# Kernel optimization log

Hardware: AMD Instinct MI355X
Metric: run time of the kernel (lower is better)

The kernel has to match this reference:

```python
import jax, jax.numpy as jnp
import numpy as np
import math

P_PARTICLES = 50
N_ITERS = 30
ROT_RANGE = math.radians(45.0)
TR_RANGE = 1.0
F_DE = 0.8
CR_DE = 0.9
SUB = 128


def axis_angle_to_rotation_matrix(v):
    # v: [..., 3] axis-angle -> [..., 3, 3] via Rodrigues formula
    theta = jnp.linalg.norm(v, axis=-1, keepdims=True)            # [..., 1]
    k = v / jnp.maximum(theta, 1e-8)
    kx, ky, kz = k[..., 0], k[..., 1], k[..., 2]
    zero = jnp.zeros_like(kx)
    K = jnp.stack([zero, -kz, ky,
                   kz, zero, -kx,
                   -ky, kx, zero], axis=-1).reshape(v.shape[:-1] + (3, 3))
    I = jnp.eye(3, dtype=v.dtype)
    s = jnp.sin(theta)[..., None]
    c = jnp.cos(theta)[..., None]
    R = I + s * K + (1.0 - c) * (K @ K)
    return jnp.where(theta[..., None] < 1e-8, I, R)


def _evaluate(src, tgt, pop):
    # src: [B,S,3] subsampled source, tgt: [B,S,3], pop: [B,P,6]
    R = axis_angle_to_rotation_matrix(pop[..., :3])               # [B,P,3,3]
    t = pop[..., 3:]                                              # [B,P,3]
    # transformed[b,p,n,k] = sum_j src[b,n,j] * R[b,p,k,j] + t[b,p,k]
    x = jnp.einsum('bnj,bpkj->bpnk', src, R) + t[:, :, None, :]   # [B,P,S,3]
    # squared-distance chamfer (symmetric, mean of nearest-neighbor dists)
    xn = jnp.sum(x * x, axis=-1)                                  # [B,P,S]
    yn = jnp.sum(tgt * tgt, axis=-1)                              # [B,S]
    cross = jnp.einsum('bpnd,bmd->bpnm', x, tgt)                  # [B,P,S,S]
    d2 = jnp.maximum(xn[..., None] + yn[:, None, None, :] - 2.0 * cross, 0.0)
    return d2.min(axis=-1).mean(axis=-1) + d2.min(axis=-2).mean(axis=-1)  # [B,P]


def setup_inputs() -> dict:
    key = jax.random.key(0)
    k1, k2 = jax.random.split(key)
    source = jax.random.normal(k1, (32, 16384, 3), dtype=jnp.float32)
    target = jax.random.normal(k2, (32, 16384, 3), dtype=jnp.float32)
    return {"source": source, "target": target}


def reference(source, target):
    B, N, _ = source.shape
    M = target.shape[1]
    P = P_PARTICLES
    key = jax.random.key(42)
    k0, k1, k2, k3, kloop = jax.random.split(key, 5)

    # subsample points for fitness evaluation (shared indices across batch)
    idx_s = jax.random.permutation(k0, N)[:SUB]
    idx_t = jax.random.permutation(k1, M)[:SUB]
    src = source[:, idx_s, :]                                     # [B,S,3]
    tgt = target[:, idx_t, :]                                     # [B,S,3]

    # init population: uniform axis-angle + translation; particle 0 = identity
    rot = jax.random.uniform(k2, (B, P, 3), minval=-ROT_RANGE, maxval=ROT_RANGE)
    tr = jax.random.uniform(k3, (B, P, 3), minval=-TR_RANGE, maxval=TR_RANGE)
    pop = jnp.concatenate([rot, tr], axis=-1).at[:, 0, :].set(0.0)
    fit = _evaluate(src, tgt, pop)                                # [B,P]

    dim_ids = jnp.arange(6)

    def step(carry, k):
        pop, fit = carry
        ka, kb, kc = jax.random.split(k, 3)
        # per-batch random permutations of particle indices (r1, r2, r3)
        perm_keys = jax.random.split(ka, 3 * B)
        perms = jax.vmap(lambda kk: jax.random.permutation(kk, P))(perm_keys)
        perms = perms.reshape(3, B, P)

        def gather(r):
            return jnp.take_along_axis(pop, r[..., None], axis=1)  # [B,P,6]

        x1, x2, x3 = gather(perms[0]), gather(perms[1]), gather(perms[2])
        mutant = x1 + F_DE * (x2 - x3)
        mutant = jnp.concatenate([
            jnp.clip(mutant[..., :3], -ROT_RANGE, ROT_RANGE),
            jnp.clip(mutant[..., 3:], -TR_RANGE, TR_RANGE),
        ], axis=-1)

        rmask = jax.random.uniform(kb, (B, P, 6)) < CR_DE
        j_rand = jax.random.randint(kc, (B, P), 0, 6)
        cross_mask = rmask | (dim_ids == j_rand[..., None])
        trial = jnp.where(cross_mask, mutant, pop)

        tfit = _evaluate(src, tgt, trial)
        improved = tfit < fit
        pop = jnp.where(improved[..., None], trial, pop)
        fit = jnp.where(improved, tfit, fit)
        return (pop, fit), None

    (pop, fit), _ = jax.lax.scan(step, (pop, fit), jax.random.split(kloop, N_ITERS))

    best_idx = jnp.argmin(fit, axis=1)                            # [B]
    best_pos = pop[jnp.arange(B), best_idx]                       # [B,6]
    R_best = axis_angle_to_rotation_matrix(best_pos[:, :3])       # [B,3,3]
    t_best = best_pos[:, 3:]                                      # [B,3]
    aligned = jnp.einsum('bnj,bkj->bnk', source, R_best) + t_best[:, None, :]
    return (R_best, t_best, aligned)
```

## Files before the change

kernel.cpp:

```cpp
#include <hip/hip_runtime.h>
#include <stdint.h>

struct U2 { unsigned a, b; };

__device__ __forceinline__ unsigned rotl32(unsigned v, int r) {
  return (v << r) | (v >> (32 - r));
}

__device__ __forceinline__ U2 tf(U2 k, unsigned x0, unsigned x1) {
  unsigned ks0 = k.a, ks1 = k.b, ks2 = k.a ^ k.b ^ 0x1BD11BDAu;
  x0 += ks0; x1 += ks1;
#define TFG(RA, RB, RC, RD, KA, KB, INC)                  \
  x0 += x1; x1 = rotl32(x1, RA); x1 ^= x0;                \
  x0 += x1; x1 = rotl32(x1, RB); x1 ^= x0;                \
  x0 += x1; x1 = rotl32(x1, RC); x1 ^= x0;                \
  x0 += x1; x1 = rotl32(x1, RD); x1 ^= x0;                \
  x0 += KA; x1 += KB + INC;
  TFG(13, 15, 26, 6, ks1, ks2, 1u)
  TFG(17, 29, 16, 24, ks2, ks0, 2u)
  TFG(13, 15, 26, 6, ks0, ks1, 3u)
  TFG(17, 29, 16, 24, ks1, ks2, 4u)
  TFG(13, 15, 26, 6, ks2, ks0, 5u)
#undef TFG
  U2 r; r.a = x0; r.b = x1; return r;
}

__device__ __forceinline__ U2 split_key(U2 key, int num, int j) {
  (void)num;
  return tf(key, 0u, (unsigned)j);
}
__device__ __forceinline__ unsigned random_bits(U2 key, int n, unsigned e) {
  (void)n;
  U2 r = tf(key, 0u, e);
  return r.a ^ r.b;
}

__device__ __forceinline__ U2 root_key() { U2 k; k.a = 0u; k.b = 42u; return k; }

__device__ __forceinline__ float jax_uniform(U2 key, int n, unsigned e,
                                             float minv, float maxv) {
  unsigned b = random_bits(key, n, e);
  float u = __uint_as_float((b >> 9) | 0x3f800000u) - 1.0f;
  float r = u * (maxv - minv) + minv;
  return fmaxf(minv, r);
}

#define ROTR 0.7853981633974483f
#define SENTINEL 0xFFFFFFFFu

__device__ __forceinline__ void compute_R(float vx, float vy, float vz,
                                          float R[3][3]) {
  float nsq = vx * vx + vy * vy + vz * vz;
  float theta = sqrtf(nsq);
  if (theta < 1e-8f) {
    R[0][0] = 1.f; R[0][1] = 0.f; R[0][2] = 0.f;
    R[1][0] = 0.f; R[1][1] = 1.f; R[1][2] = 0.f;
    R[2][0] = 0.f; R[2][1] = 0.f; R[2][2] = 1.f;
    return;
  }
  float m = fmaxf(theta, 1e-8f);
  float kx = vx / m, ky = vy / m, kz = vz / m;
  float s = sinf(theta), c = cosf(theta);
  float K[3][3] = {{0.f, -kz, ky}, {kz, 0.f, -kx}, {-ky, kx, 0.f}};
  float K2[3][3];
#pragma unroll
  for (int i = 0; i < 3; i++)
#pragma unroll
    for (int j = 0; j < 3; j++)
      K2[i][j] = fmaf(K[i][2], K[2][j], fmaf(K[i][1], K[1][j], K[i][0] * K[0][j]));
  float omc = 1.0f - c;
#pragma unroll
  for (int i = 0; i < 3; i++)
#pragma unroll
    for (int j = 0; j < 3; j++)
      R[i][j] = ((i == j) ? 1.0f : 0.0f) + s * K[i][j] + omc * K2[i][j];
}

__device__ __forceinline__ unsigned long long make_composite(int s, int i) {
  U2 root = root_key();
  U2 kp = split_key(root, 5, s >> 1);
  U2 key;
  if ((s & 1) == 0) {
    key = split_key(kp, 2, 1);
  } else {
    U2 kA = split_key(kp, 2, 0);
    key = split_key(kA, 2, 1);
  }
  unsigned rb = random_bits(key, 16384, (unsigned)i);
  return ((unsigned long long)rb << 32) | (unsigned)i;
}

__device__ __forceinline__ float gload(const float* p) {
  return __hip_atomic_load(const_cast<float*>(p), __ATOMIC_RELAXED,
                           __HIP_MEMORY_SCOPE_AGENT);
}
__device__ __forceinline__ void gstore(float* p, float v) {
  __hip_atomic_store(p, v, __ATOMIC_RELAXED, __HIP_MEMORY_SCOPE_AGENT);
}
__device__ __forceinline__ unsigned uload(const unsigned* p) {
  return __hip_atomic_load(const_cast<unsigned*>(p), __ATOMIC_RELAXED,
                           __HIP_MEMORY_SCOPE_AGENT);
}

__device__ __forceinline__ float poll_word(const float* p) {
  const unsigned* up = (const unsigned*)p;
  unsigned v = uload(up);
  while (v == SENTINEL) v = uload(up);
  return __uint_as_float(v);
}

__global__ __launch_bounds__(256) void hist_kernel(unsigned* __restrict__ hist) {
  int gid = blockIdx.x * 256 + threadIdx.x;
  int s = gid >> 14, i = gid & 16383;
  unsigned long long c = make_composite(s, i);
  unsigned bucket = (unsigned)(c >> 56);
  atomicAdd(&hist[s * 256 + bucket], 1u);
}

__global__ __launch_bounds__(256) void prefix_kernel(
    const unsigned* __restrict__ hist, unsigned* __restrict__ base,
    unsigned* __restrict__ cursor) {
  __shared__ unsigned h[4][256];
  int t = threadIdx.x;
#pragma unroll
  for (int s = 0; s < 4; s++) h[s][t] = hist[s * 256 + t];
  __syncthreads();
#pragma unroll
  for (int s = 0; s < 4; s++) {
    unsigned acc = 0;
    for (int j = 0; j < 256; j++) acc += (j < t) ? h[s][j] : 0u;
    base[s * 256 + t] = acc;
    cursor[s * 256 + t] = acc;
  }
}

__global__ __launch_bounds__(256) void scatterb_kernel(
    unsigned* __restrict__ cursor, unsigned long long* __restrict__ sorted) {
  int gid = blockIdx.x * 256 + threadIdx.x;
  int s = gid >> 14, i = gid & 16383;
  unsigned long long c = make_composite(s, i);
  unsigned bucket = (unsigned)(c >> 56);
  unsigned pos = atomicAdd(&cursor[s * 256 + bucket], 1u);
  sorted[(s << 14) + pos] = c;
}

__global__ __launch_bounds__(256) void rank_kernel(
    const unsigned long long* __restrict__ sorted,
    const unsigned* __restrict__ base, const unsigned* __restrict__ hist,
    unsigned* __restrict__ rank_all, unsigned* __restrict__ x1buf) {
  int gid = blockIdx.x * 256 + threadIdx.x;
  int s = gid >> 14, k = gid & 16383;
  unsigned long long c = sorted[(s << 14) + k];
  unsigned bucket = (unsigned)(c >> 56);
  unsigned b0 = base[s * 256 + bucket];
  unsigned cnt = hist[s * 256 + bucket];
  unsigned less = 0;
  for (unsigned j = 0; j < cnt; j++)
    less += (sorted[(s << 14) + b0 + j] < c) ? 1u : 0u;
  unsigned i = (unsigned)(c & 0xffffffffull);
  unsigned rank = b0 + less;
  if ((s & 1) == 0) x1buf[((s >> 1) << 14) + rank] = i;
  else              rank_all[(s << 14) + i] = rank;
}

__global__ __launch_bounds__(256) void idx_kernel(
    const unsigned* __restrict__ rank_all, const unsigned* __restrict__ x1buf,
    int* __restrict__ idx) {
  int gid = blockIdx.x * 256 + threadIdx.x;
  int perm = gid >> 14, i = gid & 16383;
  unsigned r = rank_all[((perm * 2 + 1) << 14) + i];
  if (r < 128u) idx[perm * 128 + (int)r] = (int)x1buf[(perm << 14) + i];
}

__global__ __launch_bounds__(128) void setupperm_kernel(
    const float* __restrict__ source, const float* __restrict__ target,
    const int* __restrict__ idx, float* __restrict__ src,
    float* __restrict__ tgt, float* __restrict__ yn,
    unsigned* __restrict__ packg) {
  int blk = blockIdx.x;
  int tid = threadIdx.x;
  if (blk < 32) {
    int b = blk;
    int is = idx[tid], it = idx[128 + tid];
#pragma unroll
    for (int d = 0; d < 3; d++)
      src[(b * 128 + tid) * 3 + d] = source[((size_t)b * 16384 + is) * 3 + d];
    float y0 = target[((size_t)b * 16384 + it) * 3 + 0];
    float y1 = target[((size_t)b * 16384 + it) * 3 + 1];
    float y2 = target[((size_t)b * 16384 + it) * 3 + 2];
    tgt[(b * 128 + tid) * 3 + 0] = y0;
    tgt[(b * 128 + tid) * 3 + 1] = y1;
    tgt[(b * 128 + tid) * 3 + 2] = y2;
    yn[b * 128 + tid] = y0 * y0 + y1 * y1 + y2 * y2;
    return;
  }
  int blk2 = blk - 32;
  int it = blk2 >> 5, b = blk2 & 31;
  __shared__ unsigned pbits[3][64];
  __shared__ int lperm[3][64];
  U2 root = root_key();
  U2 kloop = split_key(root, 5, 4);
  U2 kit = split_key(kloop, 30, it);
  U2 ka = split_key(kit, 3, 0);
  for (int e = tid; e < 150; e += 128) {
    int r = e / 50, q = e % 50;
    U2 pk = split_key(ka, 96, r * 32 + b);
    U2 sub = split_key(pk, 2, 1);
    pbits[r][q] = random_bits(sub, 50, (unsigned)q);
  }
  __syncthreads();
  for (int e = tid; e < 150; e += 128) {
    int r = e / 50, q = e % 50;
    unsigned bq = pbits[r][q];
    int cnt = 0;
    for (int j = 0; j < 50; j++) {
      unsigned bj = pbits[r][j];
      cnt += (bj < bq || (bj == bq && j < q)) ? 1 : 0;
    }
    lperm[r][cnt] = q;
  }
  __syncthreads();
  if (tid < 50) {
    int p = tid, bp = b * 50 + p;
    U2 kb = split_key(kit, 3, 1);
    U2 kc = split_key(kit, 3, 2);
    U2 kc1 = split_key(kc, 2, 0), kc2 = split_key(kc, 2, 1);
    unsigned hb = random_bits(kc1, 1600, (unsigned)bp);
    unsigned lb = random_bits(kc2, 1600, (unsigned)bp);
    int jr = (int)((((hb % 6u) * 4u) + (lb % 6u)) % 6u);
    unsigned mask = 0;
#pragma unroll
    for (int d = 0; d < 6; d++) {
      unsigned rb = random_bits(kb, 9600, (unsigned)(bp * 6 + d));
      float u = __uint_as_float((rb >> 9) | 0x3f800000u) - 1.0f;
      if ((u < 0.9f) || (d == jr)) mask |= (1u << d);
    }
    unsigned pack = (unsigned)lperm[0][p] | ((unsigned)lperm[1][p] << 6) |
                    ((unsigned)lperm[2][p] << 12) | (mask << 18);
    packg[(it * 32 + b) * 50 + p] = pack;
  }
}

__device__ __forceinline__ float eval_pose_core(
    float p0, float p1, float p2, float p3, float p4, float p5,
    float s0, float s1, float s2, int tid, const float4* syv, float4* xsv,
    float* rowpart, float* red1, float* red2) {
  float Rm[3][3];
  compute_R(p0, p1, p2, Rm);
  float x0 = fmaf(Rm[0][2], s2, fmaf(Rm[0][1], s1, Rm[0][0] * s0)) + p3;
  float x1 = fmaf(Rm[1][2], s2, fmaf(Rm[1][1], s1, Rm[1][0] * s0)) + p4;
  float x2 = fmaf(Rm[2][2], s2, fmaf(Rm[2][1], s1, Rm[2][0] * s0)) + p5;
  float xn = x0 * x0 + x1 * x1 + x2 * x2;
  xsv[tid] = make_float4(x0, x1, x2, xn);
  __syncthreads();
  int rg = tid & 31, cq = tid >> 5;
  float4 xr0 = xsv[4 * rg + 0];
  float4 xr1 = xsv[4 * rg + 1];
  float4 xr2 = xsv[4 * rg + 2];
  float4 xr3 = xsv[4 * rg + 3];
  float racc0 = 3.402823466e38f, racc1 = 3.402823466e38f;
  float racc2 = 3.402823466e38f, racc3 = 3.402823466e38f;
  float cacc[32];
#pragma unroll
  for (int cj = 0; cj < 32; cj++) {
    float4 y = syv[(cq << 5) + cj];
    float cr0 = fmaf(xr0.z, y.z, fmaf(xr0.y, y.y, xr0.x * y.x));
    float d0 = (xr0.w + y.w) - 2.0f * cr0; d0 = fmaxf(d0, 0.0f);
    float cr1 = fmaf(xr1.z, y.z, fmaf(xr1.y, y.y, xr1.x * y.x));
    float d1 = (xr1.w + y.w) - 2.0f * cr1; d1 = fmaxf(d1, 0.0f);
    float cr2 = fmaf(xr2.z, y.z, fmaf(xr2.y, y.y, xr2.x * y.x));
    float d2_ = (xr2.w + y.w) - 2.0f * cr2; d2_ = fmaxf(d2_, 0.0f);
    float cr3 = fmaf(xr3.z, y.z, fmaf(xr3.y, y.y, xr3.x * y.x));
    float d3 = (xr3.w + y.w) - 2.0f * cr3; d3 = fmaxf(d3, 0.0f);
    racc0 = fminf(racc0, d0); racc1 = fminf(racc1, d1);
    racc2 = fminf(racc2, d2_); racc3 = fminf(racc3, d3);
    cacc[cj] = fminf(fminf(d0, d1), fminf(d2_, d3));
  }
  rowpart[cq * 128 + 4 * rg + 0] = racc0;
  rowpart[cq * 128 + 4 * rg + 1] = racc1;
  rowpart[cq * 128 + 4 * rg + 2] = racc2;
  rowpart[cq * 128 + 4 * rg + 3] = racc3;
#pragma unroll
  for (int m = 16; m >= 1; m >>= 1) {
    bool hi = (rg & m) != 0;
#pragma unroll
    for (int j = 0; j < m; j++) {
      float lo_v = cacc[j], hi_v = cacc[j + m];
      float mine = hi ? hi_v : lo_v;
      float send = hi ? lo_v : hi_v;
      float recv = __shfl_xor(send, m, 64);
      cacc[j] = fminf(mine, recv);
    }
  }
  float colmin = cacc[0];
  __syncthreads();
  float rv = rowpart[tid];
  rv = fminf(rv, rowpart[128 + tid]);
  rv = fminf(rv, rowpart[256 + tid]);
  rv = fminf(rv, rowpart[384 + tid]);
  red1[tid] = rv;
  red2[tid] = colmin;
  __syncthreads();
  int l = tid & 63;
  float v1 = red1[l] + red1[l + 64];
  float v2 = red2[l] + red2[l + 64];
#pragma unroll
  for (int m = 32; m >= 1; m >>= 1) {
    v1 += __shfl_xor(v1, m, 64);
    v2 += __shfl_xor(v2, m, 64);
  }
  return v1 * 0.0078125f + v2 * 0.0078125f;
}

__device__ __forceinline__ float pop0_val(int b, int r, int d) {
  if (r == 0) return 0.0f;
  U2 root = root_key();
  unsigned ridx = (unsigned)((b * 50 + r) * 3 + (d % 3));
  if (d < 3) {
    U2 k2 = split_key(root, 5, 2);
    return jax_uniform(k2, 4800, ridx, -ROTR, ROTR);
  }
  U2 k3 = split_key(root, 5, 3);
  return jax_uniform(k3, 4800, ridx, -1.0f, 1.0f);
}

__global__ __launch_bounds__(128, 4) void de_loop_kernel(
    const float* __restrict__ srcb, const float* __restrict__ tgtb,
    const float* __restrict__ ynb, const unsigned* __restrict__ packg,
    float* __restrict__ estate, const float* __restrict__ source,
    float* __restrict__ out) {
  int blk = blockIdx.x;
  int b = blk / 50, p = blk % 50;
  int bp = blk;
  int tid = threadIdx.x;
  __shared__ float strial[8];
  __shared__ float pv4[4][6];
  __shared__ float4 syv[128];
  __shared__ float4 xsv[128];
  __shared__ float rowpart[512];
  __shared__ float red1[128];
  __shared__ float red2[128];
  __shared__ float fl[52];
  __shared__ float Rsh2[12];

  {
    float y0 = tgtb[(b * 128 + tid) * 3 + 0];
    float y1 = tgtb[(b * 128 + tid) * 3 + 1];
    float y2 = tgtb[(b * 128 + tid) * 3 + 2];
    syv[tid] = make_float4(y0, y1, y2, ynb[b * 128 + tid]);
  }
  float s0 = srcb[(b * 128 + tid) * 3 + 0];
  float s1 = srcb[(b * 128 + tid) * 3 + 1];
  float s2 = srcb[(b * 128 + tid) * 3 + 2];

  float own_f = 0.0f;
  float own_e = 0.0f;

  unsigned pack_next = packg[(0 * 32 + b) * 50 + p];

  for (int it = 0; it < 30; it++) {
    unsigned pack = pack_next;
    if (it < 29) pack_next = packg[((it + 1) * 32 + b) * 50 + p];
    int i1 = (int)(pack & 63u);
    int i2 = (int)((pack >> 6) & 63u);
    int i3 = (int)((pack >> 12) & 63u);
    unsigned mask = (pack >> 18) & 63u;

    if (it == 0) {
      if (tid < 24) {
        int u = tid / 6, d = tid % 6;
        int rows[4] = {p, i1, i2, i3};
        pv4[u][d] = pop0_val(b, rows[u], d);
      }
      __syncthreads();
      float f0 = eval_pose_core(pv4[0][0], pv4[0][1], pv4[0][2], pv4[0][3],
                                pv4[0][4], pv4[0][5],
                                s0, s1, s2, tid, syv, xsv, rowpart, red1, red2);
      if (tid < 6) {
        int d = tid;
        float mu = pv4[1][d] + 0.8f * (pv4[2][d] - pv4[3][d]);
        if (d < 3) mu = fminf(fmaxf(mu, -ROTR), ROTR);
        else       mu = fminf(fmaxf(mu, -1.0f), 1.0f);
        float pv = pv4[0][d];
        float tv = ((mask >> d) & 1u) ? mu : pv;
        strial[d] = tv;
      }
      __syncthreads();
      float tf0 = eval_pose_core(strial[0], strial[1], strial[2], strial[3],
                                 strial[4], strial[5],
                                 s0, s1, s2, tid, syv, xsv, rowpart, red1, red2);
      bool imp = tf0 < f0;
      own_f = imp ? tf0 : f0;
      if (tid < 6) own_e = imp ? strial[tid] : pv4[0][tid];
    } else {
      if (tid < 6) {
        int d = tid;
        const float* eb = &estate[((size_t)(it - 1) * 1600 + b * 50) * 8];
        const unsigned* pa = (const unsigned*)&eb[i1 * 8 + d];
        const unsigned* pb = (const unsigned*)&eb[i2 * 8 + d];
        const unsigned* pc = (const unsigned*)&eb[i3 * 8 + d];
        unsigned va = uload(pa), vb = uload(pb), vc = uload(pc);
        while (va == SENTINEL || vb == SENTINEL || vc == SENTINEL) {
          va = uload(pa); vb = uload(pb); vc = uload(pc);
        }
        float x1v = __uint_as_float(va);
        float x2v = __uint_as_float(vb);
        float x3v = __uint_as_float(vc);
        float mu = x1v + 0.8f * (x2v - x3v);
        if (d < 3) mu = fminf(fmaxf(mu, -ROTR), ROTR);
        else       mu = fminf(fmaxf(mu, -1.0f), 1.0f);
        float tv = ((mask >> d) & 1u) ? mu : own_e;
        strial[d] = tv;
      }
      __syncthreads();
      float tfv = eval_pose_core(strial[0], strial[1], strial[2], strial[3],
                                 strial[4], strial[5],
                                 s0, s1, s2, tid, syv, xsv, rowpart, red1, red2);
      bool imp = tfv < own_f;
      own_f = imp ? tfv : own_f;
      if (tid < 6) own_e = imp ? strial[tid] : own_e;
    }

    float* slot = &estate[((size_t)it * 1600 + bp) * 8];
    if (tid < 6)       gstore(&slot[tid], own_e);
    else if (tid == 6) gstore(&slot[6], own_f);
  }

  if (tid < 50) {
    fl[tid] = poll_word(&estate[((size_t)29 * 1600 + b * 50 + tid) * 8 + 6]);
  }
  __syncthreads();
  if (tid == 0) {
    int bi = 0;
    float best = fl[0];
    for (int q = 1; q < 50; q++)
      if (fl[q] < best) { best = fl[q]; bi = q; }
    const float* ep = &estate[((size_t)29 * 1600 + b * 50 + bi) * 8];
    float v[6];
#pragma unroll
    for (int d = 0; d < 6; d++) v[d] = poll_word(&ep[d]);
    float R[3][3];
    compute_R(v[0], v[1], v[2], R);
#pragma unroll
    for (int i = 0; i < 3; i++)
#pragma unroll
      for (int j = 0; j < 3; j++) Rsh2[i * 3 + j] = R[i][j];
    Rsh2[9] = v[3]; Rsh2[10] = v[4]; Rsh2[11] = v[5];
    if (p == 0) {
#pragma unroll
      for (int e = 0; e < 9; e++) out[b * 9 + e] = Rsh2[e];
      out[288 + b * 3 + 0] = v[3];
      out[288 + b * 3 + 1] = v[4];
      out[288 + b * 3 + 2] = v[5];
    }
  }
  __syncthreads();

  for (int k = p * 128 + tid; k < 16384; k += 6400) {
    size_t gid = (size_t)b * 16384 + k;
    float a0s = source[gid * 3 + 0];
    float a1s = source[gid * 3 + 1];
    float a2s = source[gid * 3 + 2];
    float a0 = fmaf(Rsh2[2], a2s, fmaf(Rsh2[1], a1s, Rsh2[0] * a0s)) + Rsh2[9];
    float a1 = fmaf(Rsh2[5], a2s, fmaf(Rsh2[4], a1s, Rsh2[3] * a0s)) + Rsh2[10];
    float a2 = fmaf(Rsh2[8], a2s, fmaf(Rsh2[7], a1s, Rsh2[6] * a0s)) + Rsh2[11];
    out[384 + gid * 3 + 0] = a0;
    out[384 + gid * 3 + 1] = a1;
    out[384 + gid * 3 + 2] = a2;
  }
}

extern "C" void kernel_launch(void* const* d_in, const int* in_sizes, int n_in,
                              void* d_out, int out_size, void* d_ws,
                              size_t ws_size, hipStream_t stream) {
  const float* source = (const float*)d_in[0];
  const float* target = (const float*)d_in[1];
  float* out = (float*)d_out;
  char* ws = (char*)d_ws;

  unsigned* packg    = (unsigned*)(ws + 0);
  float* srcb        = (float*)(ws + 192000);
  float* tgtb        = (float*)(ws + 241152);
  float* ynb         = (float*)(ws + 290304);
  int* idx           = (int*)(ws + 306688);
  unsigned* hist     = (unsigned*)(ws + 307712);
  unsigned* basep    = (unsigned*)(ws + 414208);
  unsigned* cursor   = (unsigned*)(ws + 418304);
  unsigned long long* sorted = (unsigned long long*)(ws + 422400);
  unsigned* rank_all = (unsigned*)(ws + 946688);
  unsigned* x1buf    = (unsigned*)(ws + 1208832);
  float* estate      = (float*)(ws + 422400);

  hipMemsetAsync(hist, 0, 4096, stream);
  hist_kernel<<<256, 256, 0, stream>>>(hist);
  prefix_kernel<<<1, 256, 0, stream>>>(hist, basep, cursor);
  scatterb_kernel<<<256, 256, 0, stream>>>(cursor, sorted);
  rank_kernel<<<256, 256, 0, stream>>>(sorted, basep, hist, rank_all, x1buf);
  idx_kernel<<<128, 256, 0, stream>>>(rank_all, x1buf, idx);
  hipMemsetAsync(estate, 0xFF, 1536000, stream);
  setupperm_kernel<<<992, 128, 0, stream>>>(source, target, idx, srcb, tgtb,
                                            ynb, packg);

  de_loop_kernel<<<1600, 128, 0, stream>>>(srcb, tgtb, ynb, packg, estate,
                                           source, out);
}
```

Before: 362.4 us.

## Double DE loop block width to 256 threads and fold estate init into setup

The per-particle DE kernel now runs 256 threads per block. Each thread covers 2 rows instead of 4 in the 128x128 chamfer tile, and one extra shuffle stage merges column minima across the two halves. This is meant to cut per-thread serial work and latency in the fitness evaluation, at the cost of more threads, more shuffles and higher occupancy demands. The separate hipMemsetAsync that fills the estate sentinel is removed, and setupperm_kernel now writes that fill to save a launch.

Measured after the change: 459.7 us. 1.27x slower.

```diff
diff --git a/kernel.cpp b/kernel.cpp
--- a/kernel.cpp
+++ b/kernel.cpp
@@ -176,9 +176,11 @@
     const float* __restrict__ source, const float* __restrict__ target,
     const int* __restrict__ idx, float* __restrict__ src,
     float* __restrict__ tgt, float* __restrict__ yn,
-    unsigned* __restrict__ packg) {
+    unsigned* __restrict__ packg, unsigned* __restrict__ ewords) {
   int blk = blockIdx.x;
   int tid = threadIdx.x;
+  for (int i = blk * 128 + tid; i < 384000; i += 126976)
+    ewords[i] = SENTINEL;
   if (blk < 32) {
     int b = blk;
     int is = idx[tid], it = idx[128 + tid];
@@ -245,21 +247,20 @@
     float p0, float p1, float p2, float p3, float p4, float p5,
     float s0, float s1, float s2, int tid, const float4* syv, float4* xsv,
     float* rowpart, float* red1, float* red2) {
-  float Rm[3][3];
-  compute_R(p0, p1, p2, Rm);
-  float x0 = fmaf(Rm[0][2], s2, fmaf(Rm[0][1], s1, Rm[0][0] * s0)) + p3;
-  float x1 = fmaf(Rm[1][2], s2, fmaf(Rm[1][1], s1, Rm[1][0] * s0)) + p4;
-  float x2 = fmaf(Rm[2][2], s2, fmaf(Rm[2][1], s1, Rm[2][0] * s0)) + p5;
-  float xn = x0 * x0 + x1 * x1 + x2 * x2;
-  xsv[tid] = make_float4(x0, x1, x2, xn);
-  __syncthreads();
-  int rg = tid & 31, cq = tid >> 5;
-  float4 xr0 = xsv[4 * rg + 0];
-  float4 xr1 = xsv[4 * rg + 1];
-  float4 xr2 = xsv[4 * rg + 2];
-  float4 xr3 = xsv[4 * rg + 3];
+  if (tid < 128) {
+    float Rm[3][3];
+    compute_R(p0, p1, p2, Rm);
+    float x0 = fmaf(Rm[0][2], s2, fmaf(Rm[0][1], s1, Rm[0][0] * s0)) + p3;
+    float x1 = fmaf(Rm[1][2], s2, fmaf(Rm[1][1], s1, Rm[1][0] * s0)) + p4;
+    float x2 = fmaf(Rm[2][2], s2, fmaf(Rm[2][1], s1, Rm[2][0] * s0)) + p5;
+    float xn = x0 * x0 + x1 * x1 + x2 * x2;
+    xsv[tid] = make_float4(x0, x1, x2, xn);
+  }
+  __syncthreads();
+  int rg = tid & 63, cq = tid >> 6;
+  float4 xr0 = xsv[2 * rg + 0];
+  float4 xr1 = xsv[2 * rg + 1];
   float racc0 = 3.402823466e38f, racc1 = 3.402823466e38f;
-  float racc2 = 3.402823466e38f, racc3 = 3.402823466e38f;
   float cacc[32];
 #pragma unroll
   for (int cj = 0; cj < 32; cj++) {
@@ -268,18 +269,14 @@
     float d0 = (xr0.w + y.w) - 2.0f * cr0; d0 = fmaxf(d0, 0.0f);
     float cr1 = fmaf(xr1.z, y.z, fmaf(xr1.y, y.y, xr1.x * y.x));
     float d1 = (xr1.w + y.w) - 2.0f * cr1; d1 = fmaxf(d1, 0.0f);
-    float cr2 = fmaf(xr2.z, y.z, fmaf(xr2.y, y.y, xr2.x * y.x));
-    float d2_ = (xr2.w + y.w) - 2.0f * cr2; d2_ = fmaxf(d2_, 0.0f);
-    float cr3 = fmaf(xr3.z, y.z, fmaf(xr3.y, y.y, xr3.x * y.x));
-    float d3 = (xr3.w + y.w) - 2.0f * cr3; d3 = fmaxf(d3, 0.0f);
     racc0 = fminf(racc0, d0); racc1 = fminf(racc1, d1);
-    racc2 = fminf(racc2, d2_); racc3 = fminf(racc3, d3);
-    cacc[cj] = fminf(fminf(d0, d1), fminf(d2_, d3));
-  }
-  rowpart[cq * 128 + 4 * rg + 0] = racc0;
-  rowpart[cq * 128 + 4 * rg + 1] = racc1;
-  rowpart[cq * 128 + 4 * rg + 2] = racc2;
-  rowpart[cq * 128 + 4 * rg + 3] = racc3;
+    cacc[cj] = fminf(d0, d1);
+  }
+  rowpart[cq * 128 + 2 * rg + 0] = racc0;
+  rowpart[cq * 128 + 2 * rg + 1] = racc1;
+#pragma unroll
+  for (int cj = 0; cj < 32; cj++)
+    cacc[cj] = fminf(cacc[cj], __shfl_xor(cacc[cj], 32, 64));
 #pragma unroll
   for (int m = 16; m >= 1; m >>= 1) {
     bool hi = (rg & m) != 0;
@@ -294,12 +291,14 @@
   }
   float colmin = cacc[0];
   __syncthreads();
-  float rv = rowpart[tid];
-  rv = fminf(rv, rowpart[128 + tid]);
-  rv = fminf(rv, rowpart[256 + tid]);
-  rv = fminf(rv, rowpart[384 + tid]);
-  red1[tid] = rv;
-  red2[tid] = colmin;
+  if (tid < 128) {
+    float rv = rowpart[tid];
+    rv = fminf(rv, rowpart[128 + tid]);
+    rv = fminf(rv, rowpart[256 + tid]);
+    rv = fminf(rv, rowpart[384 + tid]);
+    red1[tid] = rv;
+  }
+  if (rg < 32) red2[cq * 32 + rg] = colmin;
   __syncthreads();
   int l = tid & 63;
   float v1 = red1[l] + red1[l + 64];
@@ -324,7 +323,7 @@
   return jax_uniform(k3, 4800, ridx, -1.0f, 1.0f);
 }
 
-__global__ __launch_bounds__(128, 4) void de_loop_kernel(
+__global__ __launch_bounds__(256, 8) void de_loop_kernel(
     const float* __restrict__ srcb, const float* __restrict__ tgtb,
     const float* __restrict__ ynb, const unsigned* __restrict__ packg,
     float* __restrict__ estate, const float* __restrict__ source,
@@ -343,15 +342,16 @@
   __shared__ float fl[52];
   __shared__ float Rsh2[12];
 
-  {
+  float s0 = 0.0f, s1 = 0.0f, s2 = 0.0f;
+  if (tid < 128) {
     float y0 = tgtb[(b * 128 + tid) * 3 + 0];
     float y1 = tgtb[(b * 128 + tid) * 3 + 1];
     float y2 = tgtb[(b * 128 + tid) * 3 + 2];
     syv[tid] = make_float4(y0, y1, y2, ynb[b * 128 + tid]);
-  }
-  float s0 = srcb[(b * 128 + tid) * 3 + 0];
-  float s1 = srcb[(b * 128 + tid) * 3 + 1];
-  float s2 = srcb[(b * 128 + tid) * 3 + 2];
+    s0 = srcb[(b * 128 + tid) * 3 + 0];
+    s1 = srcb[(b * 128 + tid) * 3 + 1];
+    s2 = srcb[(b * 128 + tid) * 3 + 2];
+  }
 
   float own_f = 0.0f;
   float own_e = 0.0f;
@@ -456,7 +456,7 @@
   }
   __syncthreads();
 
-  for (int k = p * 128 + tid; k < 16384; k += 6400) {
+  for (int k = p * 256 + tid; k < 16384; k += 12800) {
     size_t gid = (size_t)b * 16384 + k;
     float a0s = source[gid * 3 + 0];
     float a1s = source[gid * 3 + 1];
@@ -497,10 +497,9 @@
   scatterb_kernel<<<256, 256, 0, stream>>>(cursor, sorted);
   rank_kernel<<<256, 256, 0, stream>>>(sorted, basep, hist, rank_all, x1buf);
   idx_kernel<<<128, 256, 0, stream>>>(rank_all, x1buf, idx);
-  hipMemsetAsync(estate, 0xFF, 1536000, stream);
   setupperm_kernel<<<992, 128, 0, stream>>>(source, target, idx, srcb, tgtb,
-                                            ynb, packg);
-
-  de_loop_kernel<<<1600, 128, 0, stream>>>(srcb, tgtb, ynb, packg, estate,
+                                            ynb, packg, (unsigned*)estate);
+
+  de_loop_kernel<<<1600, 256, 0, stream>>>(srcb, tgtb, ynb, packg, estate,
                                            source, out);
 }
```
